# Performance work log

Hardware: AMD Instinct MI355X
Metric: run time of the kernel (lower is better)

The kernel has to match this reference:

```python
import jax, jax.numpy as jnp
import numpy as np

B, C, H, W = 4, 64, 64, 64
CQK = C // 8


def setup_inputs() -> dict:
    key = jax.random.key(0)
    ks = jax.random.split(key, 4)
    x = jax.random.normal(ks[0], (B, C, H, W), dtype=jnp.float32)
    Wq = jax.random.normal(ks[1], (CQK, C), dtype=jnp.float32) * (1.0 / np.sqrt(C))
    bq = jnp.zeros((CQK,), dtype=jnp.float32)
    Wk = jax.random.normal(ks[2], (CQK, C), dtype=jnp.float32) * (1.0 / np.sqrt(C))
    bk = jnp.zeros((CQK,), dtype=jnp.float32)
    Wv = jax.random.normal(ks[3], (C, C), dtype=jnp.float32) * (1.0 / np.sqrt(C))
    bv = jnp.zeros((C,), dtype=jnp.float32)
    gamma = jnp.ones((1,), dtype=jnp.float32)
    return {"x": x, "Wq": Wq, "bq": bq, "Wk": Wk, "bk": bk,
            "Wv": Wv, "bv": bv, "gamma": gamma}


def reference(x, Wq, bq, Wk, bk, Wv, bv, gamma):
    b, c, h, w = x.shape
    n = h * w
    xf = x.reshape(b, c, n)                      # [B, C, N]
    # 1x1 convs == per-pixel linear over channels
    q = jnp.einsum('oc,bcn->bon', Wq, xf) + bq[:, None]   # [B, C/8, N]
    k = jnp.einsum('oc,bcn->bon', Wk, xf) + bk[:, None]   # [B, C/8, N]
    v = jnp.einsum('oc,bcn->bon', Wv, xf) + bv[:, None]   # [B, C, N]
    # attention_map[b,i,j] = <q[:, i], k[:, j]>; softmax over j
    attn = jax.nn.softmax(jnp.einsum('bci,bcj->bij', q, k), axis=-1)  # [B, N, N]
    # out[b,c,i] = sum_j v[b,c,j] * attn[b,i,j]  (bmm(V, attn^T))
    out = jnp.einsum('bcj,bij->bci', v, attn).reshape(b, c, h, w)
    return gamma * out + x
```

## Files before the change

kernel.cpp:

```cpp
#include <hip/hip_runtime.h>
#include <hip/hip_bf16.h>
#include <math.h>

#define NPIX 4096

typedef __attribute__((ext_vector_type(8))) short s8;
typedef __attribute__((ext_vector_type(4))) short s4;
typedef __attribute__((ext_vector_type(16))) float f16v;

static __device__ __forceinline__ unsigned packbf2(float a, float b) {
    union { __hip_bfloat162 h; unsigned u; } x;
    x.h = __float22bfloat162_rn(make_float2(a, b));
    return x.u;
}
static __device__ __forceinline__ float2 unpackbf2(unsigned u) {
    float lo = __uint_as_float(u << 16);
    float hi = __uint_as_float(u & 0xffff0000u);
    return make_float2(lo, hi);
}

__global__ __launch_bounds__(256) void prep_kernel(
    const float* __restrict__ x,
    const float* __restrict__ Wq, const float* __restrict__ bq,
    const float* __restrict__ Wk, const float* __restrict__ bk,
    __hip_bfloat16* __restrict__ qbf, __hip_bfloat16* __restrict__ kbf,
    __hip_bfloat16* __restrict__ xbf)
{
    __shared__ float Xp[64][65];
    int t = threadIdx.x;
    int lane = t & 63;
    int grp  = t >> 6;
    int b  = blockIdx.x >> 6;
    int n0 = (blockIdx.x & 63) << 6;

    const float* xb = x + ((size_t)b << 18);
    __hip_bfloat16* xbb = xbf + ((size_t)b << 18);
#pragma unroll
    for (int u = 0; u < 16; ++u) {
        int c = grp + u * 4;
        float v = xb[((size_t)c << 12) + n0 + lane];
        Xp[c][lane] = v;
        xbb[((size_t)c << 12) + n0 + lane] = __float2bfloat16(v);
    }
    __syncthreads();

    int o0 = grp * 2, o1 = o0 + 1;
    float qa0 = bq[o0], qa1 = bq[o1], ka0 = bk[o0], ka1 = bk[o1];
    const float* wq0 = Wq + o0 * 64; const float* wq1 = Wq + o1 * 64;
    const float* wk0 = Wk + o0 * 64; const float* wk1 = Wk + o1 * 64;
#pragma unroll
    for (int c = 0; c < 64; ++c) {
        float xv = Xp[c][lane];
        qa0 = fmaf(wq0[c], xv, qa0);
        qa1 = fmaf(wq1[c], xv, qa1);
        ka0 = fmaf(wk0[c], xv, ka0);
        ka1 = fmaf(wk1[c], xv, ka1);
    }
    qa0 *= 1.4426950408889634f;
    qa1 *= 1.4426950408889634f;
    int pix = b * NPIX + n0 + lane;
    *(__hip_bfloat162*)(qbf + (size_t)pix * 8 + o0) =
        __float22bfloat162_rn(make_float2(qa0, qa1));
    *(__hip_bfloat162*)(kbf + (size_t)pix * 8 + o0) =
        __float22bfloat162_rn(make_float2(ka0, ka1));
}

__global__ __launch_bounds__(512, 4) void flash_part_kernel(
    const __hip_bfloat16* __restrict__ qbf, const __hip_bfloat16* __restrict__ kbf,
    const __hip_bfloat16* __restrict__ xbf,
    __hip_bfloat16* __restrict__ Opart, float* __restrict__ Lp)
{
    __shared__ __align__(16) char pool[35840];

    int t = threadIdx.x;
    int w    = t >> 6;
    int lane = t & 63;
    int l32  = lane & 31;
    int lh   = lane >> 5;
    int g    = w >> 2;
    int sw   = w & 3;

    int blk  = blockIdx.x;
    int sId  = blk >> 8;
    int rest = blk & 255;
    int b    = rest >> 6;
    int i0   = (rest & 63) << 6;
    int jbase = sId << 10;

    const s8 zero8 = {0, 0, 0, 0, 0, 0, 0, 0};

    s8 qf;
    {
        s8 qv = *(const s8*)(qbf + ((size_t)(b * NPIX + i0 + g * 32 + l32) << 3));
        qf = (lh == 0) ? qv : zero8;
    }

    f16v acc[2];
    f16v zero16;
#pragma unroll
    for (int r = 0; r < 16; ++r) { acc[0][r] = 0.f; acc[1][r] = 0.f; zero16[r] = 0.f; }
    float lsum = 0.f;

    const __hip_bfloat16* kb = kbf + ((size_t)(b * NPIX) << 3);
    const unsigned short* xg = (const unsigned short*)xbf + ((size_t)b << 18);

    int c = t >> 3, seg = t & 7;
    const unsigned short* xsrc = xg + ((size_t)c << 12) + seg * 16;
    int xdst = c * 140 + seg * 16;

    uint2 sv0, sv1, sv2, sv3;
    s8 kf;
    {
        const unsigned short* p = xsrc + jbase;
        sv0 = *(const uint2*)(p);     sv1 = *(const uint2*)(p + 4);
        sv2 = *(const uint2*)(p + 8); sv3 = *(const uint2*)(p + 12);
        kf = *(const s8*)(kb + ((size_t)(jbase + sw * 32 + l32) << 3));
    }

    int bufp = 0;
    for (int tile = 0; tile < 8; ++tile) {
        unsigned short* Xb = (unsigned short*)(pool + bufp * 17920);

        *(uint2*)(Xb + xdst + 0)  = sv0;
        *(uint2*)(Xb + xdst + 4)  = sv1;
        *(uint2*)(Xb + xdst + 8)  = sv2;
        *(uint2*)(Xb + xdst + 12) = sv3;

        f16v sC = __builtin_amdgcn_mfma_f32_32x32x16_bf16(kf, qf, zero16, 0, 0, 0);
        float e[16];
#pragma unroll
        for (int r = 0; r < 16; ++r) e[r] = exp2f(sC[r]);
#pragma unroll
        for (int r = 0; r < 16; ++r) lsum += e[r];
        unsigned P2[8];
#pragma unroll
        for (int s = 0; s < 8; ++s) P2[s] = packbf2(e[2 * s], e[2 * s + 1]);

        {
            int jn = jbase + (((tile + 1) & 7) << 7);
            const unsigned short* p = xsrc + jn;
            sv0 = *(const uint2*)(p);     sv1 = *(const uint2*)(p + 4);
            sv2 = *(const uint2*)(p + 8); sv3 = *(const uint2*)(p + 12);
            kf = *(const s8*)(kb + ((size_t)(jn + sw * 32 + l32) << 3));
        }

        __syncthreads();

#if __has_builtin(__builtin_amdgcn_mfma_f32_32x32x8bf16_1k)
#pragma unroll
        for (int cm = 0; cm < 2; ++cm) {
            const unsigned short* xrow = Xb + (cm * 32 + l32) * 140 + sw * 32 + lh * 4;
#pragma unroll
            for (int q = 0; q < 4; ++q) {
                s4 xf = *(const s4*)(xrow + q * 8);
                union { uint2 u; s4 v; } pu;
                pu.u.x = P2[2 * q]; pu.u.y = P2[2 * q + 1];
                acc[cm] = __builtin_amdgcn_mfma_f32_32x32x8bf16_1k(xf, pu.v, acc[cm], 0, 0, 0);
            }
        }
#else
        {
            unsigned X0 = __shfl_xor(P2[0], 32), X1 = __shfl_xor(P2[1], 32);
            unsigned X2 = __shfl_xor(P2[2], 32), X3 = __shfl_xor(P2[3], 32);
            unsigned X4 = __shfl_xor(P2[4], 32), X5 = __shfl_xor(P2[5], 32);
            unsigned X6 = __shfl_xor(P2[6], 32), X7 = __shfl_xor(P2[7], 32);
            union { uint4 u[2]; s8 v[2]; } bf;
            bf.u[0].x = lh ? X2 : P2[0]; bf.u[0].y = lh ? X3 : P2[1];
            bf.u[0].z = lh ? P2[2] : X0; bf.u[0].w = lh ? P2[3] : X1;
            bf.u[1].x = lh ? X6 : P2[4]; bf.u[1].y = lh ? X7 : P2[5];
            bf.u[1].z = lh ? P2[6] : X4; bf.u[1].w = lh ? P2[7] : X5;
#pragma unroll
            for (int cm = 0; cm < 2; ++cm) {
                const unsigned short* xrow = Xb + (cm * 32 + l32) * 140 + sw * 32 + lh * 8;
#pragma unroll
                for (int q = 0; q < 2; ++q) {
                    union { uint2 u[2]; s8 v; } xu;
                    xu.u[0] = *(const uint2*)(xrow + q * 16);
                    xu.u[1] = *(const uint2*)(xrow + q * 16 + 4);
                    acc[cm] = __builtin_amdgcn_mfma_f32_32x32x16_bf16(xu.v, bf.v[q], acc[cm], 0, 0, 0);
                }
            }
        }
#endif
        bufp ^= 1;
    }

    float* Osh = (float*)pool;
    float* Lsh = (float*)(pool + 35840 - 1024);

    lsum += __shfl_xor(lsum, 32);

    __syncthreads();
    if (lh == 0) Lsh[w * 32 + l32] = lsum;

    float* OshG = Osh + g * 2176;
    for (int s = 0; s < 4; ++s) {
        __syncthreads();
        if (sw == s) {
#pragma unroll
            for (int cm = 0; cm < 2; ++cm)
#pragma unroll
                for (int r = 0; r < 16; ++r) {
                    int cc = cm * 32 + (r & 3) + 8 * (r >> 2) + 4 * lh;
                    float* p = OshG + l32 * 68 + cc;
                    if (s == 0) *p = acc[cm][r];
                    else        *p += acc[cm][r];
                }
        }
    }
    __syncthreads();

    if (t < 64) {
        int gi = t, gg = gi >> 5, ii = gi & 31;
        Lp[(size_t)blk * 64 + gi] =
            Lsh[(gg * 4 + 0) * 32 + ii] + Lsh[(gg * 4 + 1) * 32 + ii] +
            Lsh[(gg * 4 + 2) * 32 + ii] + Lsh[(gg * 4 + 3) * 32 + ii];
    }

    {
        int i = t >> 3, c0 = (t & 7) << 3;
        const float* src = Osh + (i >> 5) * 2176 + (i & 31) * 68 + c0;
        uint4 pk;
        pk.x = packbf2(src[0], src[1]); pk.y = packbf2(src[2], src[3]);
        pk.z = packbf2(src[4], src[5]); pk.w = packbf2(src[6], src[7]);
        *(uint4*)(Opart + (size_t)blk * 4096 + i * 64 + c0) = pk;
    }
}

__global__ __launch_bounds__(256) void merge_kernel(
    const __hip_bfloat16* __restrict__ Opart, const float* __restrict__ Lp,
    const float* __restrict__ Wv, const float* __restrict__ bv,
    const float* __restrict__ x, const float* __restrict__ gamma,
    float* __restrict__ out)
{
    __shared__ float Osh[32 * 68];
    __shared__ float Wvs[4096];
    __shared__ float LinvS[32];
    __shared__ float bvs[64];

    int t = threadIdx.x;
    int m  = blockIdx.x;
    int b  = m >> 7;
    int i0 = (m & 127) << 5;

    if (t < 32) {
        int gi = i0 + t;
        int fb = b * 64 + (gi >> 6);
        int r  = gi & 63;
        float lt = Lp[(size_t)(0 * 256 + fb) * 64 + r]
                 + Lp[(size_t)(1 * 256 + fb) * 64 + r]
                 + Lp[(size_t)(2 * 256 + fb) * 64 + r]
                 + Lp[(size_t)(3 * 256 + fb) * 64 + r];
        LinvS[t] = 1.0f / lt;
    }
    if (t < 64) bvs[t] = bv[t];
    {
        const float4* wsrc = (const float4*)Wv;
        float4* wdst = (float4*)Wvs;
#pragma unroll
        for (int u = 0; u < 4; ++u) wdst[t + u * 256] = wsrc[t + u * 256];
    }
    __syncthreads();

    {
        int i = t >> 3, c0 = (t & 7) << 3;
        int gi = i0 + i;
        int fb = b * 64 + (gi >> 6);
        int r  = gi & 63;
        float o[8];
#pragma unroll
        for (int k = 0; k < 8; ++k) o[k] = 0.f;
#pragma unroll
        for (int sId = 0; sId < 4; ++sId) {
            size_t base = (size_t)(sId * 256 + fb) * 4096 + r * 64 + c0;
            uint4 pk = *(const uint4*)(Opart + base);
            float2 e0 = unpackbf2(pk.x), e1 = unpackbf2(pk.y);
            float2 e2 = unpackbf2(pk.z), e3 = unpackbf2(pk.w);
            o[0] += e0.x; o[1] += e0.y; o[2] += e1.x; o[3] += e1.y;
            o[4] += e2.x; o[5] += e2.y; o[6] += e3.x; o[7] += e3.y;
        }
        float* dst = Osh + i * 68 + c0;
        *(float4*)(dst + 0) = make_float4(o[0], o[1], o[2], o[3]);
        *(float4*)(dst + 4) = make_float4(o[4], o[5], o[6], o[7]);
    }
    __syncthreads();

    {
        int i  = t & 31;
        int cg = t >> 5;
        float inv = LinvS[i];
        float res[8];
#pragma unroll
        for (int k = 0; k < 8; ++k) res[k] = 0.f;
#pragma unroll 4
        for (int cb = 0; cb < 16; ++cb) {
            float4 o = *(const float4*)(Osh + i * 68 + cb * 4);
#pragma unroll
            for (int k = 0; k < 8; ++k) {
                float4 wv4 = *(const float4*)(Wvs + (cg * 8 + k) * 64 + cb * 4);
                res[k] = fmaf(wv4.x, o.x, fmaf(wv4.y, o.y, fmaf(wv4.z, o.z, fmaf(wv4.w, o.w, res[k]))));
            }
        }
        float g = gamma[0];
        const float* xr = x + ((size_t)b << 18) + i0;
        float* outp = out + ((size_t)b << 18) + i0;
#pragma unroll
        for (int k = 0; k < 8; ++k) {
            int cch = cg * 8 + k;
            float attn = fmaf(res[k], inv, bvs[cch]);
            size_t off = ((size_t)cch << 12) + i;
            outp[off] = fmaf(g, attn, xr[off]);
        }
    }
}

extern "C" void kernel_launch(void* const* d_in, const int* in_sizes, int n_in,
                              void* d_out, int out_size, void* d_ws, size_t ws_size,
                              hipStream_t stream) {
    const float* x     = (const float*)d_in[0];
    const float* Wq    = (const float*)d_in[1];
    const float* bq    = (const float*)d_in[2];
    const float* Wk    = (const float*)d_in[3];
    const float* bk    = (const float*)d_in[4];
    const float* Wv    = (const float*)d_in[5];
    const float* bv    = (const float*)d_in[6];
    const float* gamma = (const float*)d_in[7];
    float* out = (float*)d_out;

    __hip_bfloat16* qbf   = (__hip_bfloat16*)d_ws;
    __hip_bfloat16* kbf   = qbf + (size_t)4 * NPIX * 8;
    __hip_bfloat16* xbf   = kbf + (size_t)4 * NPIX * 8;
    __hip_bfloat16* Opart = xbf + (size_t)4 * NPIX * 64;
    float* Lp = (float*)(Opart + (size_t)1024 * 4096);

    prep_kernel<<<256, 256, 0, stream>>>(x, Wq, bq, Wk, bk, qbf, kbf, xbf);
    flash_part_kernel<<<1024, 512, 0, stream>>>(qbf, kbf, xbf, Opart, Lp);
    merge_kernel<<<512, 256, 0, stream>>>(Opart, Lp, Wv, bv, x, gamma, out);
}
```

Baseline: 109.7 us.

## Fuse split-K merge into flash kernel via last-block atomic ticket

```diff
diff --git a/kernel.cpp b/kernel.cpp
--- a/kernel.cpp
+++ b/kernel.cpp
@@ -17,6 +17,13 @@
     float lo = __uint_as_float(u << 16);
     float hi = __uint_as_float(u & 0xffff0000u);
     return make_float2(lo, hi);
+}
+static __device__ __forceinline__ float fexp2(float x) {
+#if __has_builtin(__builtin_amdgcn_exp2f)
+    return __builtin_amdgcn_exp2f(x);
+#else
+    return exp2f(x);
+#endif
 }
 
 __global__ __launch_bounds__(256) void prep_kernel(
@@ -68,9 +75,13 @@
 __global__ __launch_bounds__(512, 4) void flash_part_kernel(
     const __hip_bfloat16* __restrict__ qbf, const __hip_bfloat16* __restrict__ kbf,
     const __hip_bfloat16* __restrict__ xbf,
-    __hip_bfloat16* __restrict__ Opart, float* __restrict__ Lp)
+    __hip_bfloat16* __restrict__ Opart, float* __restrict__ Lp,
+    const float* __restrict__ Wv, const float* __restrict__ bv,
+    const float* __restrict__ x, const float* __restrict__ gamma,
+    float* __restrict__ out, int* __restrict__ counters)
 {
     __shared__ __align__(16) char pool[35840];
+    __shared__ int ticket;
 
     int t = threadIdx.x;
     int w    = t >> 6;
@@ -129,7 +140,7 @@
         f16v sC = __builtin_amdgcn_mfma_f32_32x32x16_bf16(kf, qf, zero16, 0, 0, 0);
         float e[16];
 #pragma unroll
-        for (int r = 0; r < 16; ++r) e[r] = exp2f(sC[r]);
+        for (int r = 0; r < 16; ++r) e[r] = fexp2(sC[r]);
 #pragma unroll
         for (int r = 0; r < 16; ++r) lsum += e[r];
         unsigned P2[8];
@@ -225,91 +236,79 @@
         pk.z = packbf2(src[4], src[5]); pk.w = packbf2(src[6], src[7]);
         *(uint4*)(Opart + (size_t)blk * 4096 + i * 64 + c0) = pk;
     }
-}
-
-__global__ __launch_bounds__(256) void merge_kernel(
-    const __hip_bfloat16* __restrict__ Opart, const float* __restrict__ Lp,
-    const float* __restrict__ Wv, const float* __restrict__ bv,
-    const float* __restrict__ x, const float* __restrict__ gamma,
-    float* __restrict__ out)
-{
-    __shared__ float Osh[32 * 68];
-    __shared__ float Wvs[4096];
-    __shared__ float LinvS[32];
-    __shared__ float bvs[64];
-
-    int t = threadIdx.x;
-    int m  = blockIdx.x;
-    int b  = m >> 7;
-    int i0 = (m & 127) << 5;
-
-    if (t < 32) {
-        int gi = i0 + t;
-        int fb = b * 64 + (gi >> 6);
-        int r  = gi & 63;
-        float lt = Lp[(size_t)(0 * 256 + fb) * 64 + r]
-                 + Lp[(size_t)(1 * 256 + fb) * 64 + r]
-                 + Lp[(size_t)(2 * 256 + fb) * 64 + r]
-                 + Lp[(size_t)(3 * 256 + fb) * 64 + r];
-        LinvS[t] = 1.0f / lt;
-    }
-    if (t < 64) bvs[t] = bv[t];
+
+    __threadfence();
+    if (t == 0) ticket = atomicAdd(&counters[rest], 1);
+    __syncthreads();
+    if (ticket != 3) return;
+    __threadfence();
+
+    float* OshM  = (float*)pool;
+    float* WvsM  = (float*)(pool + 17408);
+    float* LinvM = (float*)(pool + 33792);
+    float* bvsM  = (float*)(pool + 34048);
+
+    if (t < 64) {
+        float lt = Lp[(size_t)(0 * 256 + rest) * 64 + t]
+                 + Lp[(size_t)(1 * 256 + rest) * 64 + t]
+                 + Lp[(size_t)(2 * 256 + rest) * 64 + t]
+                 + Lp[(size_t)(3 * 256 + rest) * 64 + t];
+        LinvM[t] = 1.0f / lt;
+        bvsM[t] = bv[t];
+    }
     {
         const float4* wsrc = (const float4*)Wv;
-        float4* wdst = (float4*)Wvs;
-#pragma unroll
-        for (int u = 0; u < 4; ++u) wdst[t + u * 256] = wsrc[t + u * 256];
+        float4* wdst = (float4*)WvsM;
+        wdst[t] = wsrc[t];
+        wdst[t + 512] = wsrc[t + 512];
     }
     __syncthreads();
 
     {
         int i = t >> 3, c0 = (t & 7) << 3;
-        int gi = i0 + i;
-        int fb = b * 64 + (gi >> 6);
-        int r  = gi & 63;
         float o[8];
 #pragma unroll
         for (int k = 0; k < 8; ++k) o[k] = 0.f;
 #pragma unroll
-        for (int sId = 0; sId < 4; ++sId) {
-            size_t base = (size_t)(sId * 256 + fb) * 4096 + r * 64 + c0;
+        for (int s2 = 0; s2 < 4; ++s2) {
+            size_t base = (size_t)(s2 * 256 + rest) * 4096 + i * 64 + c0;
             uint4 pk = *(const uint4*)(Opart + base);
             float2 e0 = unpackbf2(pk.x), e1 = unpackbf2(pk.y);
             float2 e2 = unpackbf2(pk.z), e3 = unpackbf2(pk.w);
             o[0] += e0.x; o[1] += e0.y; o[2] += e1.x; o[3] += e1.y;
             o[4] += e2.x; o[5] += e2.y; o[6] += e3.x; o[7] += e3.y;
         }
-        float* dst = Osh + i * 68 + c0;
+        float* dst = OshM + i * 68 + c0;
         *(float4*)(dst + 0) = make_float4(o[0], o[1], o[2], o[3]);
         *(float4*)(dst + 4) = make_float4(o[4], o[5], o[6], o[7]);
     }
     __syncthreads();
 
     {
-        int i  = t & 31;
-        int cg = t >> 5;
-        float inv = LinvS[i];
+        int i  = t & 63;
+        int cg = t >> 6;
+        float inv = LinvM[i];
         float res[8];
 #pragma unroll
         for (int k = 0; k < 8; ++k) res[k] = 0.f;
 #pragma unroll 4
         for (int cb = 0; cb < 16; ++cb) {
-            float4 o = *(const float4*)(Osh + i * 68 + cb * 4);
+            float4 o = *(const float4*)(OshM + i * 68 + cb * 4);
 #pragma unroll
             for (int k = 0; k < 8; ++k) {
-                float4 wv4 = *(const float4*)(Wvs + (cg * 8 + k) * 64 + cb * 4);
+                float4 wv4 = *(const float4*)(WvsM + (cg * 8 + k) * 64 + cb * 4);
                 res[k] = fmaf(wv4.x, o.x, fmaf(wv4.y, o.y, fmaf(wv4.z, o.z, fmaf(wv4.w, o.w, res[k]))));
             }
         }
-        float g = gamma[0];
+        float gam = gamma[0];
         const float* xr = x + ((size_t)b << 18) + i0;
         float* outp = out + ((size_t)b << 18) + i0;
 #pragma unroll
         for (int k = 0; k < 8; ++k) {
             int cch = cg * 8 + k;
-            float attn = fmaf(res[k], inv, bvs[cch]);
+            float attn = fmaf(res[k], inv, bvsM[cch]);
             size_t off = ((size_t)cch << 12) + i;
-            outp[off] = fmaf(g, attn, xr[off]);
+            outp[off] = fmaf(gam, attn, xr[off]);
         }
     }
 }
@@ -332,8 +331,10 @@
     __hip_bfloat16* xbf   = kbf + (size_t)4 * NPIX * 8;
     __hip_bfloat16* Opart = xbf + (size_t)4 * NPIX * 64;
     float* Lp = (float*)(Opart + (size_t)1024 * 4096);
-
+    int* counters = (int*)(Lp + 1024 * 64);
+
+    hipMemsetAsync(counters, 0, 256 * sizeof(int), stream);
     prep_kernel<<<256, 256, 0, stream>>>(x, Wq, bq, Wk, bk, qbf, kbf, xbf);
-    flash_part_kernel<<<1024, 512, 0, stream>>>(qbf, kbf, xbf, Opart, Lp);
-    merge_kernel<<<512, 256, 0, stream>>>(Opart, Lp, Wv, bv, x, gamma, out);
-}
+    flash_part_kernel<<<1024, 512, 0, stream>>>(qbf, kbf, xbf, Opart, Lp,
+                                                Wv, bv, x, gamma, out, counters);
+}
```

Result: slower. 290.2 us (+164.7%).

## Fuse flash attention with merge/projection, drop split-K partials

Applied to the files above, without the earlier changes.

```diff
diff --git a/kernel.cpp b/kernel.cpp
--- a/kernel.cpp
+++ b/kernel.cpp
@@ -13,10 +13,12 @@
     x.h = __float22bfloat162_rn(make_float2(a, b));
     return x.u;
 }
-static __device__ __forceinline__ float2 unpackbf2(unsigned u) {
-    float lo = __uint_as_float(u << 16);
-    float hi = __uint_as_float(u & 0xffff0000u);
-    return make_float2(lo, hi);
+static __device__ __forceinline__ float fexp2(float x) {
+#if __has_builtin(__builtin_amdgcn_exp2f)
+    return __builtin_amdgcn_exp2f(x);
+#else
+    return exp2f(x);
+#endif
 }
 
 __global__ __launch_bounds__(256) void prep_kernel(
@@ -65,33 +67,30 @@
         __float22bfloat162_rn(make_float2(ka0, ka1));
 }
 
-__global__ __launch_bounds__(512, 4) void flash_part_kernel(
+__global__ __launch_bounds__(512, 4) void flash_fused_kernel(
     const __hip_bfloat16* __restrict__ qbf, const __hip_bfloat16* __restrict__ kbf,
     const __hip_bfloat16* __restrict__ xbf,
-    __hip_bfloat16* __restrict__ Opart, float* __restrict__ Lp)
+    const float* __restrict__ Wv, const float* __restrict__ bv,
+    const float* __restrict__ x, const float* __restrict__ gamma,
+    float* __restrict__ out)
 {
-    __shared__ __align__(16) char pool[35840];
+    __shared__ __align__(16) char pool[35200];
+    unsigned short* Xs = (unsigned short*)pool;
 
     int t = threadIdx.x;
     int w    = t >> 6;
     int lane = t & 63;
     int l32  = lane & 31;
     int lh   = lane >> 5;
-    int g    = w >> 2;
-    int sw   = w & 3;
-
-    int blk  = blockIdx.x;
-    int sId  = blk >> 8;
-    int rest = blk & 255;
-    int b    = rest >> 6;
-    int i0   = (rest & 63) << 6;
-    int jbase = sId << 10;
+
+    int b  = blockIdx.x >> 7;
+    int i0 = (blockIdx.x & 127) << 5;
 
     const s8 zero8 = {0, 0, 0, 0, 0, 0, 0, 0};
 
     s8 qf;
     {
-        s8 qv = *(const s8*)(qbf + ((size_t)(b * NPIX + i0 + g * 32 + l32) << 3));
+        s8 qv = *(const s8*)(qbf + ((size_t)(b * NPIX + i0 + l32) << 3));
         qf = (lh == 0) ? qv : zero8;
     }
 
@@ -105,51 +104,51 @@
     const unsigned short* xg = (const unsigned short*)xbf + ((size_t)b << 18);
 
     int c = t >> 3, seg = t & 7;
-    const unsigned short* xsrc = xg + ((size_t)c << 12) + seg * 16;
-    int xdst = c * 140 + seg * 16;
-
-    uint2 sv0, sv1, sv2, sv3;
+    const unsigned short* xsrc = xg + ((size_t)c << 12) + seg * 32;
+    int xdst = c * 260 + seg * 32;
+
+    uint2 pv[8];
     s8 kf;
     {
-        const unsigned short* p = xsrc + jbase;
-        sv0 = *(const uint2*)(p);     sv1 = *(const uint2*)(p + 4);
-        sv2 = *(const uint2*)(p + 8); sv3 = *(const uint2*)(p + 12);
-        kf = *(const s8*)(kb + ((size_t)(jbase + sw * 32 + l32) << 3));
-    }
-
-    int bufp = 0;
-    for (int tile = 0; tile < 8; ++tile) {
-        unsigned short* Xb = (unsigned short*)(pool + bufp * 17920);
-
-        *(uint2*)(Xb + xdst + 0)  = sv0;
-        *(uint2*)(Xb + xdst + 4)  = sv1;
-        *(uint2*)(Xb + xdst + 8)  = sv2;
-        *(uint2*)(Xb + xdst + 12) = sv3;
+        const unsigned short* p = xsrc;
+#pragma unroll
+        for (int u = 0; u < 8; ++u) pv[u] = *(const uint2*)(p + u * 4);
+        kf = *(const s8*)(kb + ((size_t)(w * 32 + l32) << 3));
+    }
+
+    for (int jt = 0; jt < 16; ++jt) {
+        __syncthreads();
+
+        {
+            unsigned short* dstp = Xs + xdst;
+#pragma unroll
+            for (int u = 0; u < 8; ++u) *(uint2*)(dstp + u * 4) = pv[u];
+        }
 
         f16v sC = __builtin_amdgcn_mfma_f32_32x32x16_bf16(kf, qf, zero16, 0, 0, 0);
         float e[16];
 #pragma unroll
-        for (int r = 0; r < 16; ++r) e[r] = exp2f(sC[r]);
+        for (int r = 0; r < 16; ++r) e[r] = fexp2(sC[r]);
 #pragma unroll
         for (int r = 0; r < 16; ++r) lsum += e[r];
         unsigned P2[8];
 #pragma unroll
         for (int s = 0; s < 8; ++s) P2[s] = packbf2(e[2 * s], e[2 * s + 1]);
 
+        __syncthreads();
+
         {
-            int jn = jbase + (((tile + 1) & 7) << 7);
+            int jn = ((jt + 1) & 15) << 8;
             const unsigned short* p = xsrc + jn;
-            sv0 = *(const uint2*)(p);     sv1 = *(const uint2*)(p + 4);
-            sv2 = *(const uint2*)(p + 8); sv3 = *(const uint2*)(p + 12);
-            kf = *(const s8*)(kb + ((size_t)(jn + sw * 32 + l32) << 3));
-        }
-
-        __syncthreads();
+#pragma unroll
+            for (int u = 0; u < 8; ++u) pv[u] = *(const uint2*)(p + u * 4);
+            kf = *(const s8*)(kb + ((size_t)(jn + w * 32 + l32) << 3));
+        }
 
 #if __has_builtin(__builtin_amdgcn_mfma_f32_32x32x8bf16_1k)
 #pragma unroll
         for (int cm = 0; cm < 2; ++cm) {
-            const unsigned short* xrow = Xb + (cm * 32 + l32) * 140 + sw * 32 + lh * 4;
+            const unsigned short* xrow = Xs + (cm * 32 + l32) * 260 + w * 32 + lh * 4;
 #pragma unroll
             for (int q = 0; q < 4; ++q) {
                 s4 xf = *(const s4*)(xrow + q * 8);
@@ -171,7 +170,7 @@
             bf.u[1].z = lh ? P2[6] : X4; bf.u[1].w = lh ? P2[7] : X5;
 #pragma unroll
             for (int cm = 0; cm < 2; ++cm) {
-                const unsigned short* xrow = Xb + (cm * 32 + l32) * 140 + sw * 32 + lh * 8;
+                const unsigned short* xrow = Xs + (cm * 32 + l32) * 260 + w * 32 + lh * 8;
 #pragma unroll
                 for (int q = 0; q < 2; ++q) {
                     union { uint2 u[2]; s8 v; } xu;
@@ -182,27 +181,28 @@
             }
         }
 #endif
-        bufp ^= 1;
-    }
-
-    float* Osh = (float*)pool;
-    float* Lsh = (float*)(pool + 35840 - 1024);
+    }
+
+    float* OshA = (float*)pool;
+    float* OshB = (float*)(pool + 8704);
+    float* Linv = (float*)(pool + 17408);
+    float* bvs  = (float*)(pool + 17536);
+    float* Wvs  = (float*)(pool + 17792);
+    float* Lsh  = (float*)(pool + 34176);
 
     lsum += __shfl_xor(lsum, 32);
-
-    __syncthreads();
     if (lh == 0) Lsh[w * 32 + l32] = lsum;
 
-    float* OshG = Osh + g * 2176;
+    float* Og = (w >> 2) ? OshB : OshA;
     for (int s = 0; s < 4; ++s) {
         __syncthreads();
-        if (sw == s) {
+        if ((w & 3) == s) {
 #pragma unroll
             for (int cm = 0; cm < 2; ++cm)
 #pragma unroll
                 for (int r = 0; r < 16; ++r) {
                     int cc = cm * 32 + (r & 3) + 8 * (r >> 2) + 4 * lh;
-                    float* p = OshG + l32 * 68 + cc;
+                    float* p = Og + l32 * 68 + cc;
                     if (s == 0) *p = acc[cm][r];
                     else        *p += acc[cm][r];
                 }
@@ -210,94 +210,34 @@
     }
     __syncthreads();
 
-    if (t < 64) {
-        int gi = t, gg = gi >> 5, ii = gi & 31;
-        Lp[(size_t)blk * 64 + gi] =
-            Lsh[(gg * 4 + 0) * 32 + ii] + Lsh[(gg * 4 + 1) * 32 + ii] +
-            Lsh[(gg * 4 + 2) * 32 + ii] + Lsh[(gg * 4 + 3) * 32 + ii];
-    }
-
-    {
-        int i = t >> 3, c0 = (t & 7) << 3;
-        const float* src = Osh + (i >> 5) * 2176 + (i & 31) * 68 + c0;
-        uint4 pk;
-        pk.x = packbf2(src[0], src[1]); pk.y = packbf2(src[2], src[3]);
-        pk.z = packbf2(src[4], src[5]); pk.w = packbf2(src[6], src[7]);
-        *(uint4*)(Opart + (size_t)blk * 4096 + i * 64 + c0) = pk;
-    }
-}
-
-__global__ __launch_bounds__(256) void merge_kernel(
-    const __hip_bfloat16* __restrict__ Opart, const float* __restrict__ Lp,
-    const float* __restrict__ Wv, const float* __restrict__ bv,
-    const float* __restrict__ x, const float* __restrict__ gamma,
-    float* __restrict__ out)
-{
-    __shared__ float Osh[32 * 68];
-    __shared__ float Wvs[4096];
-    __shared__ float LinvS[32];
-    __shared__ float bvs[64];
-
-    int t = threadIdx.x;
-    int m  = blockIdx.x;
-    int b  = m >> 7;
-    int i0 = (m & 127) << 5;
-
     if (t < 32) {
-        int gi = i0 + t;
-        int fb = b * 64 + (gi >> 6);
-        int r  = gi & 63;
-        float lt = Lp[(size_t)(0 * 256 + fb) * 64 + r]
-                 + Lp[(size_t)(1 * 256 + fb) * 64 + r]
-                 + Lp[(size_t)(2 * 256 + fb) * 64 + r]
-                 + Lp[(size_t)(3 * 256 + fb) * 64 + r];
-        LinvS[t] = 1.0f / lt;
+        float lt = 0.f;
+#pragma unroll
+        for (int ww = 0; ww < 8; ++ww) lt += Lsh[ww * 32 + t];
+        Linv[t] = 1.0f / lt;
     }
     if (t < 64) bvs[t] = bv[t];
     {
         const float4* wsrc = (const float4*)Wv;
         float4* wdst = (float4*)Wvs;
-#pragma unroll
-        for (int u = 0; u < 4; ++u) wdst[t + u * 256] = wsrc[t + u * 256];
-    }
-    __syncthreads();
-
-    {
-        int i = t >> 3, c0 = (t & 7) << 3;
-        int gi = i0 + i;
-        int fb = b * 64 + (gi >> 6);
-        int r  = gi & 63;
-        float o[8];
-#pragma unroll
-        for (int k = 0; k < 8; ++k) o[k] = 0.f;
-#pragma unroll
-        for (int sId = 0; sId < 4; ++sId) {
-            size_t base = (size_t)(sId * 256 + fb) * 4096 + r * 64 + c0;
-            uint4 pk = *(const uint4*)(Opart + base);
-            float2 e0 = unpackbf2(pk.x), e1 = unpackbf2(pk.y);
-            float2 e2 = unpackbf2(pk.z), e3 = unpackbf2(pk.w);
-            o[0] += e0.x; o[1] += e0.y; o[2] += e1.x; o[3] += e1.y;
-            o[4] += e2.x; o[5] += e2.y; o[6] += e3.x; o[7] += e3.y;
-        }
-        float* dst = Osh + i * 68 + c0;
-        *(float4*)(dst + 0) = make_float4(o[0], o[1], o[2], o[3]);
-        *(float4*)(dst + 4) = make_float4(o[4], o[5], o[6], o[7]);
+        wdst[t] = wsrc[t];
+        wdst[t + 512] = wsrc[t + 512];
     }
     __syncthreads();
 
     {
         int i  = t & 31;
         int cg = t >> 5;
-        float inv = LinvS[i];
-        float res[8];
-#pragma unroll
-        for (int k = 0; k < 8; ++k) res[k] = 0.f;
+        float inv = Linv[i];
+        float res[4] = {0.f, 0.f, 0.f, 0.f};
 #pragma unroll 4
         for (int cb = 0; cb < 16; ++cb) {
-            float4 o = *(const float4*)(Osh + i * 68 + cb * 4);
-#pragma unroll
-            for (int k = 0; k < 8; ++k) {
-                float4 wv4 = *(const float4*)(Wvs + (cg * 8 + k) * 64 + cb * 4);
+            float4 oa = *(const float4*)(OshA + i * 68 + cb * 4);
+            float4 ob = *(const float4*)(OshB + i * 68 + cb * 4);
+            float4 o = make_float4(oa.x + ob.x, oa.y + ob.y, oa.z + ob.z, oa.w + ob.w);
+#pragma unroll
+            for (int k = 0; k < 4; ++k) {
+                const float4 wv4 = *(const float4*)(Wvs + (cg * 4 + k) * 64 + cb * 4);
                 res[k] = fmaf(wv4.x, o.x, fmaf(wv4.y, o.y, fmaf(wv4.z, o.z, fmaf(wv4.w, o.w, res[k]))));
             }
         }
@@ -305,8 +245,8 @@
         const float* xr = x + ((size_t)b << 18) + i0;
         float* outp = out + ((size_t)b << 18) + i0;
 #pragma unroll
-        for (int k = 0; k < 8; ++k) {
-            int cch = cg * 8 + k;
+        for (int k = 0; k < 4; ++k) {
+            int cch = cg * 4 + k;
             float attn = fmaf(res[k], inv, bvs[cch]);
             size_t off = ((size_t)cch << 12) + i;
             outp[off] = fmaf(g, attn, xr[off]);
@@ -327,13 +267,10 @@
     const float* gamma = (const float*)d_in[7];
     float* out = (float*)d_out;
 
-    __hip_bfloat16* qbf   = (__hip_bfloat16*)d_ws;
-    __hip_bfloat16* kbf   = qbf + (size_t)4 * NPIX * 8;
-    __hip_bfloat16* xbf   = kbf + (size_t)4 * NPIX * 8;
-    __hip_bfloat16* Opart = xbf + (size_t)4 * NPIX * 64;
-    float* Lp = (float*)(Opart + (size_t)1024 * 4096);
+    __hip_bfloat16* qbf = (__hip_bfloat16*)d_ws;
+    __hip_bfloat16* kbf = qbf + (size_t)4 * NPIX * 8;
+    __hip_bfloat16* xbf = kbf + (size_t)4 * NPIX * 8;
 
     prep_kernel<<<256, 256, 0, stream>>>(x, Wq, bq, Wk, bk, qbf, kbf, xbf);
-    flash_part_kernel<<<1024, 512, 0, stream>>>(qbf, kbf, xbf, Opart, Lp);
-    merge_kernel<<<512, 256, 0, stream>>>(Opart, Lp, Wv, bv, x, gamma, out);
-}
+    flash_fused_kernel<<<512, 512, 0, stream>>>(qbf, kbf, xbf, Wv, bv, x, gamma, out);
+}
```

After: 108.0 us. No clear change (-1.5%).
